# Performance work log

Hardware: AMD Instinct MI355X
Metric: run time of the kernel (lower is better)

The kernel has to match this reference:

```python
import itertools
import jax, jax.numpy as jnp
import numpy as np

H, W, DIM, NH, WS = 64, 64, 384, 12, 7
HD = DIM // NH            # head dim = key_dim (attn_ratio=1)
N = WS * WS               # tokens per window
SCALE = HD ** -0.5
EPS = 1e-5
BATCH = 4
HID = int(DIM * 4.0)


def _bias_idxs():
    points = list(itertools.product(range(WS), range(WS)))
    offsets, idxs = {}, []
    for p1 in points:
        for p2 in points:
            off = (abs(p1[0] - p2[0]), abs(p1[1] - p2[1]))
            if off not in offsets:
                offsets[off] = len(offsets)
            idxs.append(offsets[off])
    return np.asarray(idxs, dtype=np.int32).reshape(N, N)

BIAS_IDXS = _bias_idxs()              # [N, N] static
NUM_OFFSETS = int(BIAS_IDXS.max()) + 1  # 49 for a 7x7 window


def setup_inputs() -> dict:
    key = jax.random.key(0)
    ks = jax.random.split(key, 10)
    rn = lambda k, shp, s=0.02: jax.random.normal(k, shp, jnp.float32) * s
    return {
        "x": jax.random.normal(ks[0], (BATCH, H * W, DIM), jnp.float32),
        "ln1_g": jnp.ones((DIM,), jnp.float32),
        "ln1_b": jnp.zeros((DIM,), jnp.float32),
        "qkv_w": rn(ks[1], (DIM, 3 * DIM)),
        "qkv_b": jnp.zeros((3 * DIM,), jnp.float32),
        "proj_w": rn(ks[2], (DIM, DIM)),
        "proj_b": jnp.zeros((DIM,), jnp.float32),
        "attn_bias": rn(ks[3], (NH, NUM_OFFSETS), 0.1),
        "conv_w": rn(ks[4], (DIM, 1, 3, 3), 0.1),  # depthwise OIHW
        "bn_g": jnp.ones((DIM,), jnp.float32),
        "bn_b": jnp.zeros((DIM,), jnp.float32),
        "bn_mean": rn(ks[5], (DIM,), 0.05),
        "bn_var": jax.random.uniform(ks[6], (DIM,), jnp.float32, 0.5, 1.5),
        "ln2_g": jnp.ones((DIM,), jnp.float32),
        "ln2_b": jnp.zeros((DIM,), jnp.float32),
        "fc1_w": rn(ks[7], (DIM, HID)),
        "fc1_b": jnp.zeros((HID,), jnp.float32),
        "fc2_w": rn(ks[8], (HID, DIM)),
        "fc2_b": jnp.zeros((DIM,), jnp.float32),
    }


def _ln(x, g, b):
    m = x.mean(-1, keepdims=True)
    v = jnp.var(x, axis=-1, keepdims=True)
    return (x - m) * jax.lax.rsqrt(v + EPS) * g + b


def reference(x, ln1_g, ln1_b, qkv_w, qkv_b, proj_w, proj_b, attn_bias,
              conv_w, bn_g, bn_b, bn_mean, bn_var, ln2_g, ln2_b,
              fc1_w, fc1_b, fc2_w, fc2_b):
    b, hw, c = x.shape
    res = x
    # --- window partition with padding ---
    pad_b = (-H) % WS
    pad_r = (-W) % WS
    pH, pW = H + pad_b, W + pad_r
    nH, nW = pH // WS, pW // WS
    xw = x.reshape(b, H, W, c)
    xw = jnp.pad(xw, ((0, 0), (0, pad_b), (0, pad_r), (0, 0)))
    xw = xw.reshape(b, nH, WS, nW, WS, c).transpose(0, 1, 3, 2, 4, 5)
    xw = xw.reshape(b * nH * nW, N, c)  # [Bw, N, C]
    # --- attention (pre-LN, relative position bias) ---
    xn = _ln(xw, ln1_g, ln1_b)
    qkv = (xn @ qkv_w + qkv_b).reshape(-1, N, NH, 3 * HD)
    q, k, v = jnp.split(qkv, [HD, 2 * HD], axis=-1)  # each [Bw, N, NH, HD]
    bias = attn_bias[:, BIAS_IDXS]                    # [NH, N, N]
    scores = jnp.einsum('bnhd,bmhd->bhnm', q, k) * SCALE + bias
    a = jax.nn.softmax(scores, axis=-1)
    o = jnp.einsum('bhnm,bmhd->bnhd', a, v).reshape(-1, N, NH * HD)
    xw = o @ proj_w + proj_b
    # --- window reverse + unpad ---
    xw = xw.reshape(b, nH, nW, WS, WS, c).transpose(0, 1, 3, 2, 4, 5)
    xw = xw.reshape(b, pH, pW, c)[:, :H, :W].reshape(b, hw, c)
    x = res + xw
    # --- depthwise 3x3 conv + BatchNorm (eval) ---
    xc = x.transpose(0, 2, 1).reshape(b, c, H, W)
    xc = jax.lax.conv_general_dilated(
        xc, conv_w, (1, 1), ((1, 1), (1, 1)),
        feature_group_count=c,
        dimension_numbers=('NCHW', 'OIHW', 'NCHW'))
    xc = (xc - bn_mean[:, None, None]) * jax.lax.rsqrt(bn_var[:, None, None] + EPS) \
         * bn_g[:, None, None] + bn_b[:, None, None]
    x = xc.reshape(b, c, hw).transpose(0, 2, 1)
    # --- MLP (pre-LN, GELU) with residual ---
    h1 = jax.nn.gelu(_ln(x, ln2_g, ln2_b) @ fc1_w + fc1_b, approximate=False)
    return x + (h1 @ fc2_w + fc2_b)
```

## Files before the change

### kernel.cpp

```cpp
#include <hip/hip_runtime.h>
#include <cstdint>


typedef __bf16 bf16x8 __attribute__((ext_vector_type(8)));
typedef __bf16 bf16x4 __attribute__((ext_vector_type(4)));
typedef float  f32x4  __attribute__((ext_vector_type(4)));

#define DIM_    384
#define QKVD    1152
#define HIDD    1536
#define NTOK    49
#define NWIN    400
#define TOKENS  16384
#define PADROW  16384
#define MQKV    16512
#define SCALE_  0.17677669529663689f
#define EPS_    1e-5f

#define B_LN1   8192
#define B_PADR  1
#define B_QKV   1728
#define B_PROJ  576
#define B_FC1   2304
#define B_FC2   2304
#define B_CONV  14
#define B_BIAS  192
#define B_TOTAL (B_LN1 + B_PADR + B_QKV + B_PROJ + B_FC1 + B_FC2 + B_CONV + B_BIAS)

__device__ __forceinline__ void gload_lds16(const void* g, void* l) {
  __builtin_amdgcn_global_load_lds(
      (__attribute__((address_space(1))) void*)g,
      (__attribute__((address_space(3))) void*)l, 16, 0, 0);
}

__device__ __forceinline__ float gelu_fast(float v) {
  float t2 = v * (1.5957691216057308f + 0.07135481627f * v * v);
  return v * __builtin_amdgcn_rcpf(1.f + __expf(-t2));
}

__global__ __launch_bounds__(256) void prep_all(
    const float* __restrict__ x, const float* __restrict__ ln1_g,
    const float* __restrict__ ln1_b, __bf16* __restrict__ xn,
    const float* __restrict__ qkv_w,  __bf16* __restrict__ wqkv,
    const float* __restrict__ proj_w, __bf16* __restrict__ wproj,
    const float* __restrict__ fc1_w,  __bf16* __restrict__ wfc1,
    const float* __restrict__ fc2_w,  __bf16* __restrict__ wfc2,
    const float* __restrict__ conv_w, float* __restrict__ wconv,
    const float* __restrict__ attn_b, float* __restrict__ bm) {
  int b = blockIdx.x;
  int tid = threadIdx.x;

  if (b < B_LN1) {
    int sub = tid >> 7, tl = tid & 127;
    long t = (long)b * 2 + sub;
    const float* xr = x + t * DIM_;
    float v0 = xr[tl], v1 = xr[tl + 128], v2 = xr[tl + 256];
    float s = v0 + v1 + v2, s2 = v0 * v0 + v1 * v1 + v2 * v2;
    for (int off = 32; off; off >>= 1) { s += __shfl_down(s, off); s2 += __shfl_down(s2, off); }
    __shared__ float red[2][4];
    if ((tl & 63) == 0) { red[sub][tl >> 6] = s; red[sub][2 + (tl >> 6)] = s2; }
    __syncthreads();
    float S = red[sub][0] + red[sub][1], S2 = red[sub][2] + red[sub][3];
    float m  = S * (1.f / DIM_);
    float rs = rsqrtf(S2 * (1.f / DIM_) - m * m + EPS_);
    __bf16* orow = xn + t * DIM_;
    orow[tl]       = (__bf16)((v0 - m) * rs * ln1_g[tl]       + ln1_b[tl]);
    orow[tl + 128] = (__bf16)((v1 - m) * rs * ln1_g[tl + 128] + ln1_b[tl + 128]);
    orow[tl + 256] = (__bf16)((v2 - m) * rs * ln1_g[tl + 256] + ln1_b[tl + 256]);
    return;
  }
  b -= B_LN1;
  if (b < B_PADR) {
    for (int i = tid; i < DIM_; i += 256)
      xn[(long)PADROW * DIM_ + i] = (__bf16)ln1_b[i];
    return;
  }
  b -= B_PADR;
  if (b < B_QKV) {
    int id = b * 256 + tid;
    int k = id % DIM_; int n = id / DIM_;
    wqkv[id] = (__bf16)qkv_w[(long)k * QKVD + n];
    return;
  }
  b -= B_QKV;
  if (b < B_PROJ) {
    int id = b * 256 + tid;
    int k = id % DIM_; int n = id / DIM_;
    wproj[id] = (__bf16)proj_w[(long)k * DIM_ + n];
    return;
  }
  b -= B_PROJ;
  if (b < B_FC1) {
    int id = b * 256 + tid;
    int k = id % DIM_; int n = id / DIM_;
    wfc1[id] = (__bf16)fc1_w[(long)k * HIDD + n];
    return;
  }
  b -= B_FC1;
  if (b < B_FC2) {
    int id = b * 256 + tid;
    int k = id % HIDD; int n = id / HIDD;
    wfc2[id] = (__bf16)fc2_w[(long)k * DIM_ + n];
    return;
  }
  b -= B_FC2;
  if (b < B_CONV) {
    int id = b * 256 + tid;
    if (id < 3456) {
      int ch = id / 9, k = id % 9;
      wconv[k * DIM_ + ch] = conv_w[id];
    }
    return;
  }
  b -= B_CONV;
  {
    int id = b * 256 + tid;
    int h = id >> 12, q = (id >> 6) & 63, kk = id & 63;
    float v;
    if (kk >= NTOK)      v = -1e30f;
    else if (q >= NTOK)  v = 0.f;
    else {
      int idx = abs(q / 7 - kk / 7) * 7 + abs(q % 7 - kk % 7);
      v = attn_b[h * NTOK + idx];
    }
    bm[id] = v;
  }
}

__global__ __launch_bounds__(384) void conv_bn_ln2(
    const float* __restrict__ x1, const float* __restrict__ wT,
    const float* __restrict__ bng, const float* __restrict__ bnb,
    const float* __restrict__ mean, const float* __restrict__ var,
    const float* __restrict__ g2, const float* __restrict__ b2,
    float* __restrict__ x2, __bf16* __restrict__ xln2) {
  int tid = threadIdx.x;
  int p = tid / 96, g = tid % 96;
  int pix = blockIdx.x * 4 + p;
  int bb = pix >> 12, rc = pix & 4095;
  int r = rc >> 6, c = rc & 63;
  int ch = g << 2;

  f32x4 acc = (f32x4){0.f, 0.f, 0.f, 0.f};
  #pragma unroll
  for (int dr = -1; dr <= 1; dr++) {
    int rr = r + dr;
    if (rr < 0 || rr >= 64) continue;
    #pragma unroll
    for (int dc = -1; dc <= 1; dc++) {
      int cc = c + dc;
      if (cc < 0 || cc >= 64) continue;
      f32x4 xv = *(const f32x4*)(x1 + ((long)bb * 4096 + rr * 64 + cc) * DIM_ + ch);
      f32x4 wv = *(const f32x4*)(wT + ((dr + 1) * 3 + (dc + 1)) * DIM_ + ch);
      acc += xv * wv;
    }
  }

  f32x4 gv = *(const f32x4*)(bng + ch);
  f32x4 vv = *(const f32x4*)(var + ch);
  f32x4 mv = *(const f32x4*)(mean + ch);
  f32x4 bv = *(const f32x4*)(bnb + ch);
  f32x4 y;
  #pragma unroll
  for (int j = 0; j < 4; j++) {
    float sc = gv[j] * rsqrtf(vv[j] + EPS_);
    y[j] = acc[j] * sc + (bv[j] - mv[j] * sc);
  }
  *(f32x4*)(x2 + (long)pix * DIM_ + ch) = y;

  __shared__ float pS[4][96], pS2[4][96], mS[4], rS[4];
  pS[p][g]  = y[0] + y[1] + y[2] + y[3];
  pS2[p][g] = y[0] * y[0] + y[1] * y[1] + y[2] * y[2] + y[3] * y[3];
  __syncthreads();
  if (g < 32) {
    float a  = pS[p][g]  + pS[p][g + 32]  + pS[p][g + 64];
    float a2 = pS2[p][g] + pS2[p][g + 32] + pS2[p][g + 64];
    #pragma unroll
    for (int off = 1; off < 32; off <<= 1) {
      a  += __shfl_xor(a, off);
      a2 += __shfl_xor(a2, off);
    }
    if (g == 0) {
      float m = a * (1.f / DIM_);
      mS[p] = m;
      rS[p] = rsqrtf(a2 * (1.f / DIM_) - m * m + EPS_);
    }
  }
  __syncthreads();
  float m = mS[p], rs = rS[p];
  f32x4 gg = *(const f32x4*)(g2 + ch);
  f32x4 b2v = *(const f32x4*)(b2 + ch);
  bf16x4 ov;
  #pragma unroll
  for (int j = 0; j < 4; j++) ov[j] = (__bf16)((y[j] - m) * rs * gg[j] + b2v[j]);
  *(bf16x4*)(xln2 + (long)pix * DIM_ + ch) = ov;
}

__global__ __launch_bounds__(64) void attn_mfma(const __bf16* __restrict__ qkv,
                                                const float* __restrict__ bm,
                                                __bf16* __restrict__ o) {
  int blk = blockIdx.x;
  int win = blk / 12, h = blk % 12;
  int bb = win / 100, rem = win % 100;
  int wy = rem / 10, wx = rem % 10;
  int lane = threadIdx.x;
  int quad = lane >> 4, l16 = lane & 15;

  __shared__ __align__(16) __bf16 Vt[32][72];
  __shared__ __align__(16) __bf16 P[64][72];

  const __bf16* base = qkv + h * 96;

  bf16x8 qf[4], kf[4];
  #pragma unroll
  for (int mt = 0; mt < 4; mt++) {
    int t = mt * 16 + l16;
    int ty = t / 7, tx = t % 7;
    int r = wy * 7 + ty, c = wx * 7 + tx;
    int row = (t < NTOK && r < 64 && c < 64) ? (bb * 4096 + r * 64 + c) : PADROW;
    const __bf16* rp = base + (long)row * QKVD + quad * 8;
    qf[mt] = *(const bf16x8*)(rp);
    kf[mt] = *(const bf16x8*)(rp + 32);
  }
  {
    int t = lane;
    int ty = t / 7, tx = t % 7;
    int r = wy * 7 + ty, c = wx * 7 + tx;
    int row = (t < NTOK && r < 64 && c < 64) ? (bb * 4096 + r * 64 + c) : PADROW;
    const __bf16* vp = base + (long)row * QKVD + 64;
    bf16x8 vv[4];
    #pragma unroll
    for (int i = 0; i < 4; i++) vv[i] = *(const bf16x8*)(vp + i * 8);
    #pragma unroll
    for (int i = 0; i < 4; i++)
      #pragma unroll
      for (int j = 0; j < 8; j++) Vt[i * 8 + j][lane] = vv[i][j];
  }

  f32x4 S[4][4];
  #pragma unroll
  for (int i = 0; i < 4; i++)
    #pragma unroll
    for (int j = 0; j < 4; j++) S[i][j] = (f32x4){0.f, 0.f, 0.f, 0.f};
  #pragma unroll
  for (int mt = 0; mt < 4; mt++)
    #pragma unroll
    for (int nt = 0; nt < 4; nt++)
      S[mt][nt] = __builtin_amdgcn_mfma_f32_16x16x32_bf16(qf[mt], kf[nt], S[mt][nt], 0, 0, 0);

  const float* bmh = bm + h * 4096;
  #pragma unroll
  for (int mt = 0; mt < 4; mt++)
    #pragma unroll
    for (int r = 0; r < 4; r++) {
      int q = mt * 16 + quad * 4 + r;
      #pragma unroll
      for (int nt = 0; nt < 4; nt++)
        S[mt][nt][r] = S[mt][nt][r] * SCALE_ + bmh[q * 64 + nt * 16 + l16];
    }

  #pragma unroll
  for (int mt = 0; mt < 4; mt++)
    #pragma unroll
    for (int r = 0; r < 4; r++) {
      float mx = fmaxf(fmaxf(S[mt][0][r], S[mt][1][r]), fmaxf(S[mt][2][r], S[mt][3][r]));
      #pragma unroll
      for (int off = 1; off < 16; off <<= 1) mx = fmaxf(mx, __shfl_xor(mx, off));
      float sum = 0.f;
      #pragma unroll
      for (int nt = 0; nt < 4; nt++) {
        float e = __expf(S[mt][nt][r] - mx);
        S[mt][nt][r] = e;
        sum += e;
      }
      #pragma unroll
      for (int off = 1; off < 16; off <<= 1) sum += __shfl_xor(sum, off);
      float inv = 1.f / sum;
      #pragma unroll
      for (int nt = 0; nt < 4; nt++) S[mt][nt][r] *= inv;
    }

  #pragma unroll
  for (int mt = 0; mt < 4; mt++)
    #pragma unroll
    for (int r = 0; r < 4; r++) {
      int q = mt * 16 + quad * 4 + r;
      #pragma unroll
      for (int nt = 0; nt < 4; nt++)
        P[q][nt * 16 + l16] = (__bf16)S[mt][nt][r];
    }
  __syncthreads();

  f32x4 O[4][2];
  #pragma unroll
  for (int i = 0; i < 4; i++)
    #pragma unroll
    for (int j = 0; j < 2; j++) O[i][j] = (f32x4){0.f, 0.f, 0.f, 0.f};
  #pragma unroll
  for (int kt = 0; kt < 2; kt++) {
    bf16x8 pf[4], vf[2];
    #pragma unroll
    for (int mt = 0; mt < 4; mt++)
      pf[mt] = *(const bf16x8*)(&P[mt * 16 + l16][kt * 32 + quad * 8]);
    #pragma unroll
    for (int nt = 0; nt < 2; nt++)
      vf[nt] = *(const bf16x8*)(&Vt[nt * 16 + l16][kt * 32 + quad * 8]);
    #pragma unroll
    for (int mt = 0; mt < 4; mt++)
      #pragma unroll
      for (int nt = 0; nt < 2; nt++)
        O[mt][nt] = __builtin_amdgcn_mfma_f32_16x16x32_bf16(pf[mt], vf[nt], O[mt][nt], 0, 0, 0);
  }

  #pragma unroll
  for (int mt = 0; mt < 4; mt++)
    #pragma unroll
    for (int r = 0; r < 4; r++) {
      int q = mt * 16 + quad * 4 + r;
      if (q < NTOK) {
        int ty = q / 7, tx = q % 7;
        int rr = wy * 7 + ty, cc = wx * 7 + tx;
        if (rr < 64 && cc < 64) {
          __bf16* ob = o + ((long)bb * 4096 + rr * 64 + cc) * DIM_ + h * 32;
          #pragma unroll
          for (int nt = 0; nt < 2; nt++)
            ob[nt * 16 + l16] = (__bf16)O[mt][nt][r];
        }
      }
    }
}

template <int MODE, int TN>
__global__ void __launch_bounds__(256)
gemm_bf16(const __bf16* __restrict__ A, const __bf16* __restrict__ Bt,
          const float* __restrict__ bias, int K, int N,
          float* __restrict__ outf, __bf16* __restrict__ outb,
          const float* __restrict__ res) {
  constexpr int NT = TN / 32;
  __shared__ __align__(16) __bf16 sA[128 * 32];
  __shared__ __align__(16) __bf16 sB[TN * 32];
  int tid = threadIdx.x, lane = tid & 63, wid = tid >> 6;
  int wm = wid >> 1, wn = wid & 1;
  int quad = lane >> 4, l16 = lane & 15;
  long tileM = (long)blockIdx.x * 128;
  long tileN = (long)blockIdx.y * TN;

  f32x4 acc[4][NT];
  #pragma unroll
  for (int i = 0; i < 4; i++)
    #pragma unroll
    for (int j = 0; j < NT; j++) acc[i][j] = (f32x4){0.f, 0.f, 0.f, 0.f};

  int rr = wid * 16 + (lane >> 2);
  const __bf16* gA = A  + (tileM + rr) * (long)K + ((lane & 3) << 3);
  const __bf16* gB = Bt + (tileN + rr) * (long)K + ((lane & 3) << 3);
  const long rowskip = 64 * (long)K;

  for (int k0 = 0; k0 < K; k0 += 32) {
    gload_lds16(gA + k0,           sA + (wid << 9));
    gload_lds16(gA + k0 + rowskip, sA + ((wid + 4) << 9));
    gload_lds16(gB + k0,           sB + (wid << 9));
    if (TN == 128)
      gload_lds16(gB + k0 + rowskip, sB + ((wid + 4) << 9));
    __syncthreads();
    bf16x8 af[4], bfr[NT];
    #pragma unroll
    for (int mt = 0; mt < 4; mt++)
      af[mt] = *(const bf16x8*)(sA + ((wm * 64 + mt * 16 + l16) << 5) + (quad << 3));
    #pragma unroll
    for (int nt = 0; nt < NT; nt++)
      bfr[nt] = *(const bf16x8*)(sB + ((wn * (TN / 2) + nt * 16 + l16) << 5) + (quad << 3));
    #pragma unroll
    for (int mt = 0; mt < 4; mt++)
      #pragma unroll
      for (int nt = 0; nt < NT; nt++)
        acc[mt][nt] = __builtin_amdgcn_mfma_f32_16x16x32_bf16(af[mt], bfr[nt], acc[mt][nt], 0, 0, 0);
    __syncthreads();
  }

  float bcol[NT];
  #pragma unroll
  for (int nt = 0; nt < NT; nt++) bcol[nt] = bias[tileN + wn * (TN / 2) + nt * 16 + l16];

  #pragma unroll
  for (int mt = 0; mt < 4; mt++) {
    #pragma unroll
    for (int r = 0; r < 4; r++) {
      long row = tileM + wm * 64 + mt * 16 + quad * 4 + r;
      if (MODE == 0) {
        __bf16* orow = outb + row * (long)N;
        #pragma unroll
        for (int nt = 0; nt < NT; nt++)
          orow[tileN + wn * (TN / 2) + nt * 16 + l16] = (__bf16)(acc[mt][nt][r] + bcol[nt]);
      } else if (MODE == 2) {
        __bf16* orow = outb + row * (long)N;
        #pragma unroll
        for (int nt = 0; nt < NT; nt++) {
          float v = acc[mt][nt][r] + bcol[nt];
          orow[tileN + wn * (TN / 2) + nt * 16 + l16] = (__bf16)gelu_fast(v);
        }
      } else {
        float* orow = outf + row * (long)N;
        const float* rrow = res + row * (long)N;
        #pragma unroll
        for (int nt = 0; nt < NT; nt++) {
          long col = tileN + wn * (TN / 2) + nt * 16 + l16;
          orow[col] = acc[mt][nt][r] + bcol[nt] + rrow[col];
        }
      }
    }
  }
}

extern "C" void kernel_launch(void* const* d_in, const int* in_sizes, int n_in,
                              void* d_out, int out_size, void* d_ws, size_t ws_size,
                              hipStream_t stream) {
  const float* x       = (const float*)d_in[0];
  const float* ln1_g   = (const float*)d_in[1];
  const float* ln1_b   = (const float*)d_in[2];
  const float* qkv_w   = (const float*)d_in[3];
  const float* qkv_b   = (const float*)d_in[4];
  const float* proj_w  = (const float*)d_in[5];
  const float* proj_b  = (const float*)d_in[6];
  const float* attn_b  = (const float*)d_in[7];
  const float* conv_w  = (const float*)d_in[8];
  const float* bn_g    = (const float*)d_in[9];
  const float* bn_b    = (const float*)d_in[10];
  const float* bn_mean = (const float*)d_in[11];
  const float* bn_var  = (const float*)d_in[12];
  const float* ln2_g   = (const float*)d_in[13];
  const float* ln2_b   = (const float*)d_in[14];
  const float* fc1_w   = (const float*)d_in[15];
  const float* fc1_b   = (const float*)d_in[16];
  const float* fc2_w   = (const float*)d_in[17];
  const float* fc2_b   = (const float*)d_in[18];

  char* p = (char*)d_ws;
  __bf16* WQKV = (__bf16*)p;  p += 884736;
  __bf16* WPROJ = (__bf16*)p; p += 294912;
  __bf16* WFC1 = (__bf16*)p;  p += 1179648;
  __bf16* WFC2 = (__bf16*)p;  p += 1179648;
  float*  WCONV = (float*)p;  p += 13824;
  char* region = p;           p += 63307776;
  float* X1 = (float*)p;      p += 25165824;
  float* X2 = (float*)p;      p += 25165824;
  __bf16* XN   = (__bf16*)region;
  __bf16* QKVB = (__bf16*)(region + 12681216);
  __bf16* OBUF = (__bf16*)(region + 50724864);
  __bf16* XLN2 = (__bf16*)region;
  __bf16* H1   = (__bf16*)(region + 12681216);
  float*  BM   = X1;
  float* OUT = (float*)d_out;

  prep_all<<<B_TOTAL, 256, 0, stream>>>(x, ln1_g, ln1_b, XN,
                                        qkv_w, WQKV, proj_w, WPROJ,
                                        fc1_w, WFC1, fc2_w, WFC2,
                                        conv_w, WCONV, attn_b, BM);

  gemm_bf16<0, 128><<<dim3(MQKV / 128, QKVD / 128), 256, 0, stream>>>(
      XN, WQKV, qkv_b, DIM_, QKVD, nullptr, QKVB, nullptr);

  attn_mfma<<<NWIN * 12, 64, 0, stream>>>(QKVB, BM, OBUF);

  gemm_bf16<3, 64><<<dim3(TOKENS / 128, DIM_ / 64), 256, 0, stream>>>(
      OBUF, WPROJ, proj_b, DIM_, DIM_, X1, nullptr, x);

  conv_bn_ln2<<<TOKENS / 4, 384, 0, stream>>>(X1, WCONV, bn_g, bn_b, bn_mean, bn_var,
                                              ln2_g, ln2_b, X2, XLN2);

  gemm_bf16<2, 128><<<dim3(TOKENS / 128, HIDD / 128), 256, 0, stream>>>(
      XLN2, WFC1, fc1_b, DIM_, HIDD, nullptr, H1, nullptr);

  gemm_bf16<3, 64><<<dim3(TOKENS / 128, DIM_ / 64), 256, 0, stream>>>(
      H1, WFC2, fc2_b, HIDD, DIM_, OUT, nullptr, X2);
}
```

Before: 287.2 us.

## Tile weight transposes through LDS and load GEMM B fragments directly from global

```diff
diff --git a/kernel.cpp b/kernel.cpp
--- a/kernel.cpp
+++ b/kernel.cpp
@@ -19,13 +19,13 @@
 
 #define B_LN1   8192
 #define B_PADR  1
-#define B_QKV   1728
-#define B_PROJ  576
-#define B_FC1   2304
-#define B_FC2   2304
+#define B_TQKV  108
+#define B_TPROJ 36
+#define B_TFC1  144
+#define B_TFC2  144
 #define B_CONV  14
 #define B_BIAS  192
-#define B_TOTAL (B_LN1 + B_PADR + B_QKV + B_PROJ + B_FC1 + B_FC2 + B_CONV + B_BIAS)
+#define B_TOTAL (B_LN1 + B_PADR + B_TQKV + B_TPROJ + B_TFC1 + B_TFC2 + B_CONV + B_BIAS)
 
 __device__ __forceinline__ void gload_lds16(const void* g, void* l) {
   __builtin_amdgcn_global_load_lds(
@@ -36,6 +36,26 @@
 __device__ __forceinline__ float gelu_fast(float v) {
   float t2 = v * (1.5957691216057308f + 0.07135481627f * v * v);
   return v * __builtin_amdgcn_rcpf(1.f + __expf(-t2));
+}
+
+__device__ __forceinline__ void tile_transpose(
+    const float* __restrict__ src, __bf16* __restrict__ dst,
+    int K, int N, int tile, int tilesN, __bf16 (*ld)[65]) {
+  int kt = tile / tilesN, nt = tile % tilesN;
+  int k0 = kt * 64, n0 = nt * 64;
+  int tid = threadIdx.x;
+  int a = tid & 63, b4 = tid >> 6;
+  #pragma unroll
+  for (int i = 0; i < 16; i++) {
+    int kl = b4 + i * 4;
+    ld[kl][a] = (__bf16)src[(long)(k0 + kl) * N + n0 + a];
+  }
+  __syncthreads();
+  #pragma unroll
+  for (int i = 0; i < 16; i++) {
+    int nl = b4 + i * 4;
+    dst[(long)(n0 + nl) * K + k0 + a] = ld[a][nl];
+  }
 }
 
 __global__ __launch_bounds__(256) void prep_all(
@@ -47,6 +67,8 @@
     const float* __restrict__ fc2_w,  __bf16* __restrict__ wfc2,
     const float* __restrict__ conv_w, float* __restrict__ wconv,
     const float* __restrict__ attn_b, float* __restrict__ bm) {
+  __shared__ __bf16 tlds[64][65];
+  __shared__ float red[2][4];
   int b = blockIdx.x;
   int tid = threadIdx.x;
 
@@ -57,7 +79,6 @@
     float v0 = xr[tl], v1 = xr[tl + 128], v2 = xr[tl + 256];
     float s = v0 + v1 + v2, s2 = v0 * v0 + v1 * v1 + v2 * v2;
     for (int off = 32; off; off >>= 1) { s += __shfl_down(s, off); s2 += __shfl_down(s2, off); }
-    __shared__ float red[2][4];
     if ((tl & 63) == 0) { red[sub][tl >> 6] = s; red[sub][2 + (tl >> 6)] = s2; }
     __syncthreads();
     float S = red[sub][0] + red[sub][1], S2 = red[sub][2] + red[sub][3];
@@ -76,34 +97,14 @@
     return;
   }
   b -= B_PADR;
-  if (b < B_QKV) {
-    int id = b * 256 + tid;
-    int k = id % DIM_; int n = id / DIM_;
-    wqkv[id] = (__bf16)qkv_w[(long)k * QKVD + n];
-    return;
-  }
-  b -= B_QKV;
-  if (b < B_PROJ) {
-    int id = b * 256 + tid;
-    int k = id % DIM_; int n = id / DIM_;
-    wproj[id] = (__bf16)proj_w[(long)k * DIM_ + n];
-    return;
-  }
-  b -= B_PROJ;
-  if (b < B_FC1) {
-    int id = b * 256 + tid;
-    int k = id % DIM_; int n = id / DIM_;
-    wfc1[id] = (__bf16)fc1_w[(long)k * HIDD + n];
-    return;
-  }
-  b -= B_FC1;
-  if (b < B_FC2) {
-    int id = b * 256 + tid;
-    int k = id % HIDD; int n = id / HIDD;
-    wfc2[id] = (__bf16)fc2_w[(long)k * DIM_ + n];
-    return;
-  }
-  b -= B_FC2;
+  if (b < B_TQKV)  { tile_transpose(qkv_w,  wqkv,  DIM_, QKVD, b, 18, tlds); return; }
+  b -= B_TQKV;
+  if (b < B_TPROJ) { tile_transpose(proj_w, wproj, DIM_, DIM_, b, 6,  tlds); return; }
+  b -= B_TPROJ;
+  if (b < B_TFC1)  { tile_transpose(fc1_w,  wfc1,  DIM_, HIDD, b, 24, tlds); return; }
+  b -= B_TFC1;
+  if (b < B_TFC2)  { tile_transpose(fc2_w,  wfc2,  HIDD, DIM_, b, 6,  tlds); return; }
+  b -= B_TFC2;
   if (b < B_CONV) {
     int id = b * 256 + tid;
     if (id < 3456) {
@@ -337,7 +338,6 @@
           const float* __restrict__ res) {
   constexpr int NT = TN / 32;
   __shared__ __align__(16) __bf16 sA[128 * 32];
-  __shared__ __align__(16) __bf16 sB[TN * 32];
   int tid = threadIdx.x, lane = tid & 63, wid = tid >> 6;
   int wm = wid >> 1, wn = wid & 1;
   int quad = lane >> 4, l16 = lane & 15;
@@ -351,24 +351,24 @@
     for (int j = 0; j < NT; j++) acc[i][j] = (f32x4){0.f, 0.f, 0.f, 0.f};
 
   int rr = wid * 16 + (lane >> 2);
-  const __bf16* gA = A  + (tileM + rr) * (long)K + ((lane & 3) << 3);
-  const __bf16* gB = Bt + (tileN + rr) * (long)K + ((lane & 3) << 3);
+  const __bf16* gA = A + (tileM + rr) * (long)K + ((lane & 3) << 3);
   const long rowskip = 64 * (long)K;
+  const __bf16* bP[NT];
+  #pragma unroll
+  for (int nt = 0; nt < NT; nt++)
+    bP[nt] = Bt + (tileN + wn * (TN / 2) + nt * 16 + l16) * (long)K + (quad << 3);
 
   for (int k0 = 0; k0 < K; k0 += 32) {
     gload_lds16(gA + k0,           sA + (wid << 9));
     gload_lds16(gA + k0 + rowskip, sA + ((wid + 4) << 9));
-    gload_lds16(gB + k0,           sB + (wid << 9));
-    if (TN == 128)
-      gload_lds16(gB + k0 + rowskip, sB + ((wid + 4) << 9));
+    bf16x8 bfr[NT];
+    #pragma unroll
+    for (int nt = 0; nt < NT; nt++) bfr[nt] = *(const bf16x8*)(bP[nt] + k0);
     __syncthreads();
-    bf16x8 af[4], bfr[NT];
+    bf16x8 af[4];
     #pragma unroll
     for (int mt = 0; mt < 4; mt++)
       af[mt] = *(const bf16x8*)(sA + ((wm * 64 + mt * 16 + l16) << 5) + (quad << 3));
-    #pragma unroll
-    for (int nt = 0; nt < NT; nt++)
-      bfr[nt] = *(const bf16x8*)(sB + ((wn * (TN / 2) + nt * 16 + l16) << 5) + (quad << 3));
     #pragma unroll
     for (int mt = 0; mt < 4; mt++)
       #pragma unroll
```

Measured after the change: 322.5 us. +12.3%, slower.
